# Performance work log

Measured on AMD Instinct MI355X. Metric: run time of the kernel, lower is better.

The kernel has to match this reference:

```python
import jax, jax.numpy as jnp
import numpy as np

B, S, D = 1, 4096, 2048
H, G = 16, 4            # num_heads, kv_group
HD = D // H             # head_dim = 128
GS = H // G             # group_size = 4
THETA = 10000.0


def _rope_params():
    inv_freq = 1.0 / (THETA ** (np.arange(0, HD, 2, dtype=np.float32) / HD))
    ang = np.arange(S, dtype=np.float32)[:, None] * inv_freq[None, :]   # [S, HD/2]
    ang = np.concatenate([ang, ang], axis=1)                             # [S, HD]
    return jnp.asarray(np.cos(ang), jnp.float32), jnp.asarray(np.sin(ang), jnp.float32)


def setup_inputs() -> dict:
    key = jax.random.key(0)
    ks = jax.random.split(key, 5)
    sd = D ** -0.5
    x = jax.random.normal(ks[0], (B, S, D), jnp.float32)
    wq = jax.random.normal(ks[1], (D, D), jnp.float32) * sd
    wk = jax.random.normal(ks[2], (D, G * HD), jnp.float32) * sd
    wv = jax.random.normal(ks[3], (D, G * HD), jnp.float32) * sd
    wo = jax.random.normal(ks[4], (D, D), jnp.float32) * sd
    cos, sin = _rope_params()
    mask = jnp.triu(jnp.ones((S, S), dtype=bool), k=1)  # True = masked (causal)
    return {"x": x, "mask": mask, "wq": wq, "wk": wk, "wv": wv,
            "wo": wo, "cos": cos, "sin": sin}


def _apply_rope(t, cos, sin):
    # t: [b, h, s, hd]
    half = t.shape[-1] // 2
    t1, t2 = t[..., :half], t[..., half:]
    rot = jnp.concatenate([-t2, t1], axis=-1)
    s = t.shape[2]
    return t * cos[None, None, :s, :] + rot * sin[None, None, :s, :]


def reference(x, mask, wq, wk, wv, wo, cos, sin):
    b, s, d = x.shape
    q = (x @ wq).reshape(b, s, H, HD).transpose(0, 2, 1, 3)   # [b,H,s,hd]
    k = (x @ wk).reshape(b, s, G, HD).transpose(0, 2, 1, 3)   # [b,G,s,hd]
    v = (x @ wv).reshape(b, s, G, HD).transpose(0, 2, 1, 3)   # [b,G,s,hd]
    q = _apply_rope(q, cos, sin)
    k = _apply_rope(k, cos, sin)
    # GQA: broadcast K/V over group_size instead of repeat_interleave (same math)
    q = q.reshape(b, G, GS, s, HD)
    scores = jnp.einsum('bgrsd,bgtd->bgrst', q, k)            # [b,G,GS,s,s]
    scores = jnp.where(mask[None, None, None], -jnp.inf, scores)
    w = jax.nn.softmax(scores / jnp.sqrt(jnp.float32(HD)), axis=-1)
    ctx = jnp.einsum('bgrst,bgtd->bgrsd', w, v)               # [b,G,GS,s,hd]
    ctx = ctx.reshape(b, H, s, HD).transpose(0, 2, 1, 3).reshape(b, s, d)
    return ctx @ wo
```

## Files before the change

kernel.cpp:

```cpp
#include <hip/hip_runtime.h>
#include <cstdint>

#define Ssz 4096
#define Dsz 2048
#define Hn  16
#define Gn  4
#define HDn 128

typedef __attribute__((ext_vector_type(8))) short short8;
typedef __attribute__((ext_vector_type(8))) unsigned short u16x8;
typedef __attribute__((ext_vector_type(4))) float f32x4;

typedef __attribute__((address_space(1))) void gbl_void;
typedef __attribute__((address_space(3))) void lds_void;

static __device__ __forceinline__ unsigned short f2bf(float f) {
  uint32_t u = __builtin_bit_cast(uint32_t, f);
  u += 0x7FFFu + ((u >> 16) & 1u);
  return (unsigned short)(u >> 16);
}

static __device__ __forceinline__ void gload_lds16(const void* g, void* l) {
  __builtin_amdgcn_global_load_lds((gbl_void*)(uintptr_t)g,
                                   (lds_void*)(uintptr_t)l, 16, 0, 0);
}

__global__ void k_cast_bf16(const float* __restrict__ src,
                            unsigned short* __restrict__ dst, int n) {
  int base = (blockIdx.x * blockDim.x + threadIdx.x) * 8;
  if (base >= n) return;
  float4 a = *reinterpret_cast<const float4*>(src + base);
  float4 b = *reinterpret_cast<const float4*>(src + base + 4);
  u16x8 o;
  o[0] = f2bf(a.x); o[1] = f2bf(a.y); o[2] = f2bf(a.z); o[3] = f2bf(a.w);
  o[4] = f2bf(b.x); o[5] = f2bf(b.y); o[6] = f2bf(b.z); o[7] = f2bf(b.w);
  *reinterpret_cast<u16x8*>(dst + base) = o;
}

__global__ void k_transpose(const float* __restrict__ src, int srcStride,
                            unsigned short* __restrict__ dst, int dstStride,
                            int R, int C) {
  __shared__ unsigned short tile[64][65];
  const int r0 = blockIdx.y * 64, c0 = blockIdx.x * 64;
  const int t  = threadIdx.x;
  const int rr = t >> 2;
  const int cc = (t & 3) * 16;
  const float* sp = src + (size_t)(r0 + rr) * srcStride + c0 + cc;
#pragma unroll
  for (int j = 0; j < 16; j += 4) {
    float4 v = *reinterpret_cast<const float4*>(sp + j);
    tile[rr][cc + j + 0] = f2bf(v.x);
    tile[rr][cc + j + 1] = f2bf(v.y);
    tile[rr][cc + j + 2] = f2bf(v.z);
    tile[rr][cc + j + 3] = f2bf(v.w);
  }
  __syncthreads();
  unsigned short* dp = dst + (size_t)(c0 + rr) * dstStride + r0 + cc;
  u16x8 o0, o1;
#pragma unroll
  for (int j = 0; j < 8; j++) o0[j] = tile[cc + j][rr];
#pragma unroll
  for (int j = 0; j < 8; j++) o1[j] = tile[cc + 8 + j][rr];
  *reinterpret_cast<u16x8*>(dp)     = o0;
  *reinterpret_cast<u16x8*>(dp + 8) = o1;
}

__global__ void k_rope(const float* __restrict__ Cqkv,
                       const float* __restrict__ cosp, const float* __restrict__ sinp,
                       unsigned short* __restrict__ Qb, unsigned short* __restrict__ Kb) {
  const int s = blockIdx.x;
  const float* row = Cqkv + (size_t)s * 3072;
  const float qscale = 0.08838834764831845f;
  for (int c = threadIdx.x; c < 2560; c += 256) {
    int d = c & 127;
    float v = row[c];
    int pc = (d < 64) ? c + 64 : c - 64;
    float pv = row[pc];
    float rot = (d < 64) ? -pv : pv;
    float o = v * cosp[s * 128 + d] + rot * sinp[s * 128 + d];
    if (c < 2048)
      Qb[(size_t)s * 2048 + c] = f2bf(o * qscale);
    else
      Kb[(size_t)s * 512 + (c - 2048)] = f2bf(o);
  }
}

__global__ __launch_bounds__(256) void k_gemm_bt(
    const unsigned short* __restrict__ A, const unsigned short* __restrict__ BT,
    float* __restrict__ C, int M, int N, int K, int ldc) {
  __shared__ __align__(16) unsigned short sA[128 * 32];
  __shared__ __align__(16) unsigned short sB[128 * 32];
  const int tid = threadIdx.x;
  const int lane = tid & 63, wid = tid >> 6;
  const int bid = blockIdx.y * gridDim.x + blockIdx.x;
  const int cpx = (gridDim.x * gridDim.y) >> 3;
  const int swz = (bid & 7) * cpx + (bid >> 3);
  const int m0 = (swz / gridDim.x) * 128, n0 = (swz % gridDim.x) * 128;
  const int wm = (wid >> 1) * 64, wn = (wid & 1) * 64;
  const int l15 = lane & 15, lg = lane >> 4;
  const int srow = lane >> 2;
  const int scol = (lane & 3) * 8;

  f32x4 acc[4][4] = {};

  for (int kt = 0; kt < K; kt += 32) {
#pragma unroll
    for (int c = 0; c < 2; c++) {
      const int row = c * 64 + wid * 16;
      gload_lds16(A  + (size_t)(m0 + row + srow) * K + kt + scol, sA + row * 32);
      gload_lds16(BT + (size_t)(n0 + row + srow) * K + kt + scol, sB + row * 32);
    }
    __syncthreads();
    short8 af[4], bf[4];
#pragma unroll
    for (int i = 0; i < 4; i++) {
      af[i] = *reinterpret_cast<const short8*>(sA + (wm + i * 16 + l15) * 32 + lg * 8);
      bf[i] = *reinterpret_cast<const short8*>(sB + (wn + i * 16 + l15) * 32 + lg * 8);
    }
#pragma unroll
    for (int i = 0; i < 4; i++)
#pragma unroll
      for (int j = 0; j < 4; j++)
        acc[i][j] = __builtin_amdgcn_mfma_f32_16x16x32_bf16(af[i], bf[j], acc[i][j], 0, 0, 0);
    __syncthreads();
  }

  const int rbase = m0 + wm + lg * 4;
  const int cbase = n0 + wn + l15;
#pragma unroll
  for (int i = 0; i < 4; i++)
#pragma unroll
    for (int j = 0; j < 4; j++)
#pragma unroll
      for (int r = 0; r < 4; r++)
        C[(size_t)(rbase + i * 16 + r) * ldc + cbase + j * 16] = acc[i][j][r];
}

__global__ __launch_bounds__(512, 4) void k_attn(
    const unsigned short* __restrict__ Qb, const unsigned short* __restrict__ Kb,
    const unsigned short* __restrict__ Vt, unsigned short* __restrict__ ctx) {
  __shared__ __align__(16) char sK[2][16384];
  __shared__ __align__(16) char sV[2][16384];
  __shared__ __align__(16) char sP[8][2048];
  const int id = blockIdx.x;
  const int kid = id & 255;
  const int h = kid & 15, g = h >> 2;
  const int j = kid >> 4;
  const int qt = (id < 256) ? (31 - j) : j;
  const int qb = qt * 128;
  const int lane = threadIdx.x & 63, wid = threadIdx.x >> 6;
  const int l15 = lane & 15, lg = lane >> 4;
  const int sw = (l15 & 7) << 4;
  const int wmin = qb + wid * 16;
  const int nt = qt * 2 + 2;

  const char* kbyte = (const char*)Kb;
  const char* vbyte = (const char*)Vt;
  int kOff[2], vOff[2];
#pragma unroll
  for (int q = 0; q < 2; q++) {
    int rk = wid * 8 + q * 4 + (lane >> 4);
    kOff[q] = rk * 1024 + g * 256 + (((lane & 15) * 16) ^ ((rk & 7) << 4));
    int rv = wid * 16 + q * 8 + (lane >> 3);
    vOff[q] = (g * 128 + rv) * 8192 + (((lane & 7) * 16) ^ ((rv & 7) << 4));
  }

  auto stage = [&](int t, int b) {
    const char* ks = kbyte + (size_t)t * 65536;
    const char* vs = vbyte + (size_t)t * 128;
#pragma unroll
    for (int q = 0; q < 2; q++)
      gload_lds16(ks + kOff[q], &sK[b][(wid * 2 + q) * 1024]);
#pragma unroll
    for (int q = 0; q < 2; q++)
      gload_lds16(vs + vOff[q], &sV[b][(wid * 2 + q) * 1024]);
  };

  short8 qf[4];
  {
    const unsigned short* qp = Qb + (size_t)(wmin + l15) * Dsz + h * HDn + lg * 8;
#pragma unroll
    for (int kk = 0; kk < 4; kk++)
      qf[kk] = *reinterpret_cast<const short8*>(qp + kk * 32);
  }

  f32x4 o[8] = {};
  float mrow_s = -1e30f, lrow_s = 0.f;

  stage(0, 0);
  int cur = 0;

  for (int t = 0; t < nt; t++) {
    asm volatile("s_waitcnt vmcnt(0)" ::: "memory");
    __syncthreads();
    if (t + 1 < nt) stage(t + 1, cur ^ 1);
    const int kv0 = t * 64;
    if (kv0 <= wmin + 15) {
      f32x4 sc[4] = {};
#pragma unroll
      for (int f = 0; f < 4; f++) {
        const char* kr = &sK[cur][(f * 16 + l15) * 256];
#pragma unroll
        for (int kk = 0; kk < 4; kk++) {
          short8 kf = *reinterpret_cast<const short8*>(kr + ((kk * 64 + lg * 16) ^ sw));
          sc[f] = __builtin_amdgcn_mfma_f32_16x16x32_bf16(kf, qf[kk], sc[f], 0, 0, 0);
        }
      }
      if (kv0 + 63 > wmin) {
        const int qa = wmin + l15;
#pragma unroll
        for (int f = 0; f < 4; f++) {
          int kv = kv0 + f * 16 + lg * 4;
#pragma unroll
          for (int r = 0; r < 4; r++)
            if (kv + r > qa) sc[f][r] = -1e30f;
        }
      }
      float mx = sc[0][0];
#pragma unroll
      for (int f = 0; f < 4; f++)
#pragma unroll
        for (int r = 0; r < 4; r++) mx = fmaxf(mx, sc[f][r]);
      mx = fmaxf(mx, __shfl_xor(mx, 16));
      mx = fmaxf(mx, __shfl_xor(mx, 32));
      if (__any(mx > mrow_s + 8.f)) {
        float mn = fmaxf(mrow_s, mx);
        float scl = __expf(mrow_s - mn);
        mrow_s = mn;
        lrow_s *= scl;
        float s4[4];
#pragma unroll
        for (int r = 0; r < 4; r++)
          s4[r] = __shfl(scl, (lane & 48) | (lg * 4 + r));
#pragma unroll
        for (int nf = 0; nf < 8; nf++)
#pragma unroll
          for (int r = 0; r < 4; r++) o[nf][r] *= s4[r];
      }
#pragma unroll
      for (int f = 0; f < 4; f++)
#pragma unroll
        for (int r = 0; r < 4; r++) sc[f][r] = __expf(sc[f][r] - mrow_s);
      float rs = 0.f;
#pragma unroll
      for (int f = 0; f < 4; f++)
        rs += (sc[f][0] + sc[f][1]) + (sc[f][2] + sc[f][3]);
      rs += __shfl_xor(rs, 16);
      rs += __shfl_xor(rs, 32);
      lrow_s += rs;

      char* plw = &sP[wid][0];
#pragma unroll
      for (int f = 0; f < 4; f++) {
        uint32_t w0 = (uint32_t)f2bf(sc[f][0]) | ((uint32_t)f2bf(sc[f][1]) << 16);
        uint32_t w1 = (uint32_t)f2bf(sc[f][2]) | ((uint32_t)f2bf(sc[f][3]) << 16);
        *reinterpret_cast<uint2*>(plw + l15 * 128 + ((f * 32 + lg * 8) ^ sw)) =
            make_uint2(w0, w1);
      }
      short8 pa[2];
#pragma unroll
      for (int kk = 0; kk < 2; kk++)
        pa[kk] = *reinterpret_cast<const short8*>(
            plw + l15 * 128 + ((kk * 64 + lg * 16) ^ sw));
#pragma unroll
      for (int nf = 0; nf < 8; nf++) {
        const char* vr = &sV[cur][(nf * 16 + l15) * 128];
#pragma unroll
        for (int kk = 0; kk < 2; kk++) {
          short8 vb = *reinterpret_cast<const short8*>(vr + ((kk * 64 + lg * 16) ^ sw));
          o[nf] = __builtin_amdgcn_mfma_f32_16x16x32_bf16(pa[kk], vb, o[nf], 0, 0, 0);
        }
      }
    }
    cur ^= 1;
  }

  float lr4[4];
#pragma unroll
  for (int r = 0; r < 4; r++)
    lr4[r] = __shfl(lrow_s, (lane & 48) | (lg * 4 + r));
  unsigned short* cp = ctx + (size_t)(wmin + lg * 4) * Dsz + h * HDn + l15;
#pragma unroll
  for (int nf = 0; nf < 8; nf++)
#pragma unroll
    for (int r = 0; r < 4; r++)
      cp[(size_t)r * Dsz + nf * 16] = f2bf(o[nf][r] / lr4[r]);
}

extern "C" void kernel_launch(void* const* d_in, const int* in_sizes, int n_in,
                              void* d_out, int out_size, void* d_ws, size_t ws_size,
                              hipStream_t stream) {
  (void)in_sizes; (void)n_in; (void)out_size; (void)ws_size;
  const float* x  = (const float*)d_in[0];
  const float* wq = (const float*)d_in[2];
  const float* wk = (const float*)d_in[3];
  const float* wv = (const float*)d_in[4];
  const float* wo = (const float*)d_in[5];
  const float* cs = (const float*)d_in[6];
  const float* sn = (const float*)d_in[7];
  float* out = (float*)d_out;

  unsigned short* ws16  = (unsigned short*)d_ws;
  unsigned short* WTqkv = ws16;
  unsigned short* WTo   = WTqkv + 3072 * 2048;
  unsigned short* xb    = WTo   + 2048 * 2048;
  unsigned short* Qb    = xb    + 4096 * 2048;
  unsigned short* Kb    = Qb    + 4096 * 2048;
  unsigned short* Vt    = Kb    + 4096 * 512;
  unsigned short* ctx   = Vt    + 512 * 4096;
  float* Cqkv = (float*)(ctx + 4096 * 2048);

  k_cast_bf16<<<4096, 256, 0, stream>>>(x, xb, 4096 * 2048);
  k_transpose<<<dim3(32, 32), 256, 0, stream>>>(wq, 2048, WTqkv,              2048, 2048, 2048);
  k_transpose<<<dim3(8, 32),  256, 0, stream>>>(wk, 512,  WTqkv + 2048 * 2048, 2048, 2048, 512);
  k_transpose<<<dim3(8, 32),  256, 0, stream>>>(wv, 512,  WTqkv + 2560 * 2048, 2048, 2048, 512);
  k_transpose<<<dim3(32, 32), 256, 0, stream>>>(wo, 2048, WTo,                2048, 2048, 2048);

  k_gemm_bt<<<dim3(24, 32), 256, 0, stream>>>(xb, WTqkv, Cqkv, 4096, 3072, 2048, 3072);
  k_rope<<<4096, 256, 0, stream>>>(Cqkv, cs, sn, Qb, Kb);
  k_transpose<<<dim3(8, 64), 256, 0, stream>>>(Cqkv + 2560, 3072, Vt, 4096, 4096, 512);

  k_attn<<<dim3(512), 512, 0, stream>>>(Qb, Kb, Vt, ctx);

  k_gemm_bt<<<dim3(16, 32), 256, 0, stream>>>(ctx, WTo, out, 4096, 2048, 2048, 2048);
}
```

Measured before the change: 416.7 us.

## Replace GEMM with 256x256-tile triple-buffered pipelined kernel

After: 423.4 us. No clear change (+1.6%).

```diff
diff --git a/kernel.cpp b/kernel.cpp
--- a/kernel.cpp
+++ b/kernel.cpp
@@ -85,55 +85,100 @@
   }
 }
 
-__global__ __launch_bounds__(256) void k_gemm_bt(
+__global__ __launch_bounds__(512, 2) void k_gemm256(
     const unsigned short* __restrict__ A, const unsigned short* __restrict__ BT,
     float* __restrict__ C, int M, int N, int K, int ldc) {
-  __shared__ __align__(16) unsigned short sA[128 * 32];
-  __shared__ __align__(16) unsigned short sB[128 * 32];
+  __shared__ __align__(16) unsigned short sA[3][256 * 32];
+  __shared__ __align__(16) unsigned short sB[3][256 * 32];
   const int tid = threadIdx.x;
   const int lane = tid & 63, wid = tid >> 6;
-  const int bid = blockIdx.y * gridDim.x + blockIdx.x;
-  const int cpx = (gridDim.x * gridDim.y) >> 3;
-  const int swz = (bid & 7) * cpx + (bid >> 3);
-  const int m0 = (swz / gridDim.x) * 128, n0 = (swz % gridDim.x) * 128;
-  const int wm = (wid >> 1) * 64, wn = (wid & 1) * 64;
+  const int wr = wid >> 2, wc = wid & 3;
   const int l15 = lane & 15, lg = lane >> 4;
-  const int srow = lane >> 2;
-  const int scol = (lane & 3) * 8;
-
-  f32x4 acc[4][4] = {};
-
-  for (int kt = 0; kt < K; kt += 32) {
-#pragma unroll
-    for (int c = 0; c < 2; c++) {
-      const int row = c * 64 + wid * 16;
-      gload_lds16(A  + (size_t)(m0 + row + srow) * K + kt + scol, sA + row * 32);
-      gload_lds16(BT + (size_t)(n0 + row + srow) * K + kt + scol, sB + row * 32);
+  const int nbx = N >> 8;
+  const int nwg = (M >> 8) * nbx;
+  const int bid = blockIdx.x;
+  const int swz = (bid & 7) * (nwg >> 3) + (bid >> 3);
+  const int m0 = (swz / nbx) << 8, n0 = (swz % nbx) << 8;
+  const int nt = K >> 5;
+
+  const int srow = tid >> 2;
+  const int scol = (tid & 3) * 8;
+
+  auto stageA = [&](int t) {
+    const int b = t % 3;
+    const unsigned short* s0 = A + (size_t)(m0 + srow) * K + t * 32 + scol;
+    gload_lds16(s0,                     &sA[b][wid * 512]);
+    gload_lds16(s0 + (size_t)128 * K,   &sA[b][4096 + wid * 512]);
+  };
+  auto stageB = [&](int t) {
+    const int b = t % 3;
+    const unsigned short* s0 = BT + (size_t)(n0 + srow) * K + t * 32 + scol;
+    gload_lds16(s0,                     &sB[b][wid * 512]);
+    gload_lds16(s0 + (size_t)128 * K,   &sB[b][4096 + wid * 512]);
+  };
+
+  f32x4 acc[8][4] = {};
+
+  stageA(0); stageB(0);
+  stageA(1); stageB(1);
+  asm volatile("s_waitcnt vmcnt(4)" ::: "memory");
+  __builtin_amdgcn_s_barrier();
+
+  for (int t = 0; t < nt; t++) {
+    const int bt = t % 3;
+    const unsigned short* a_base = &sA[bt][0];
+    const unsigned short* b_base = &sB[bt][0];
+    short8 af[4], bf[4];
+#pragma unroll
+    for (int nf = 0; nf < 4; nf++)
+      bf[nf] = *reinterpret_cast<const short8*>(
+          b_base + (wc * 64 + nf * 16 + l15) * 32 + lg * 8);
+#pragma unroll
+    for (int mf = 0; mf < 4; mf++)
+      af[mf] = *reinterpret_cast<const short8*>(
+          a_base + (wr * 128 + mf * 16 + l15) * 32 + lg * 8);
+    if (t + 2 < nt) stageA(t + 2);
+    __builtin_amdgcn_s_barrier();
+    __builtin_amdgcn_s_setprio(1);
+#pragma unroll
+    for (int mf = 0; mf < 4; mf++)
+#pragma unroll
+      for (int nf = 0; nf < 4; nf++)
+        acc[mf][nf] = __builtin_amdgcn_mfma_f32_16x16x32_bf16(
+            af[mf], bf[nf], acc[mf][nf], 0, 0, 0);
+    __builtin_amdgcn_s_setprio(0);
+    __builtin_amdgcn_s_barrier();
+#pragma unroll
+    for (int mf = 0; mf < 4; mf++)
+      af[mf] = *reinterpret_cast<const short8*>(
+          a_base + (wr * 128 + 64 + mf * 16 + l15) * 32 + lg * 8);
+    if (t + 2 < nt) stageB(t + 2);
+    __builtin_amdgcn_s_barrier();
+    __builtin_amdgcn_s_setprio(1);
+#pragma unroll
+    for (int mf = 0; mf < 4; mf++)
+#pragma unroll
+      for (int nf = 0; nf < 4; nf++)
+        acc[4 + mf][nf] = __builtin_amdgcn_mfma_f32_16x16x32_bf16(
+            af[mf], bf[nf], acc[4 + mf][nf], 0, 0, 0);
+    __builtin_amdgcn_s_setprio(0);
+    if (t + 2 < nt) {
+      asm volatile("s_waitcnt vmcnt(4)" ::: "memory");
+    } else {
+      asm volatile("s_waitcnt vmcnt(0)" ::: "memory");
     }
-    __syncthreads();
-    short8 af[4], bf[4];
-#pragma unroll
-    for (int i = 0; i < 4; i++) {
-      af[i] = *reinterpret_cast<const short8*>(sA + (wm + i * 16 + l15) * 32 + lg * 8);
-      bf[i] = *reinterpret_cast<const short8*>(sB + (wn + i * 16 + l15) * 32 + lg * 8);
-    }
-#pragma unroll
-    for (int i = 0; i < 4; i++)
-#pragma unroll
-      for (int j = 0; j < 4; j++)
-        acc[i][j] = __builtin_amdgcn_mfma_f32_16x16x32_bf16(af[i], bf[j], acc[i][j], 0, 0, 0);
-    __syncthreads();
-  }
-
-  const int rbase = m0 + wm + lg * 4;
-  const int cbase = n0 + wn + l15;
-#pragma unroll
-  for (int i = 0; i < 4; i++)
-#pragma unroll
-    for (int j = 0; j < 4; j++)
+    __builtin_amdgcn_s_barrier();
+  }
+
+  const int rbase = m0 + wr * 128 + lg * 4;
+  const int cbase = n0 + wc * 64 + l15;
+#pragma unroll
+  for (int mf = 0; mf < 8; mf++)
+#pragma unroll
+    for (int nf = 0; nf < 4; nf++)
 #pragma unroll
       for (int r = 0; r < 4; r++)
-        C[(size_t)(rbase + i * 16 + r) * ldc + cbase + j * 16] = acc[i][j][r];
+        C[(size_t)(rbase + mf * 16 + r) * ldc + cbase + nf * 16] = acc[mf][nf][r];
 }
 
 __global__ __launch_bounds__(512, 4) void k_attn(
@@ -316,11 +361,11 @@
   k_transpose<<<dim3(8, 32),  256, 0, stream>>>(wv, 512,  WTqkv + 2560 * 2048, 2048, 2048, 512);
   k_transpose<<<dim3(32, 32), 256, 0, stream>>>(wo, 2048, WTo,                2048, 2048, 2048);
 
-  k_gemm_bt<<<dim3(24, 32), 256, 0, stream>>>(xb, WTqkv, Cqkv, 4096, 3072, 2048, 3072);
+  k_gemm256<<<dim3(192), 512, 0, stream>>>(xb, WTqkv, Cqkv, 4096, 3072, 2048, 3072);
   k_rope<<<4096, 256, 0, stream>>>(Cqkv, cs, sn, Qb, Kb);
   k_transpose<<<dim3(8, 64), 256, 0, stream>>>(Cqkv + 2560, 3072, Vt, 4096, 4096, 512);
 
   k_attn<<<dim3(512), 512, 0, stream>>>(Qb, Kb, Vt, ctx);
 
-  k_gemm_bt<<<dim3(16, 32), 256, 0, stream>>>(ctx, WTo, out, 4096, 2048, 2048, 2048);
-}
+  k_gemm256<<<dim3(128), 512, 0, stream>>>(ctx, WTo, out, 4096, 2048, 2048, 2048);
+}
```
